# Kernel optimization log

Measured on AMD Instinct MI355X. Metric: run time of the kernel, lower is better.

The kernel has to match this reference:

```python
import jax, jax.numpy as jnp
import numpy as np

N_ATOM_BASIS = 128
MAX_Z = 100
N_GAUSSIANS = 25
N_FILTERS = 128
R_CUTOFF = 5.0


def ssp(x):
    # shifted softplus: log(0.5*exp(x) + 0.5)
    return jax.nn.softplus(x) - jnp.log(2.0).astype(x.dtype)


def setup_inputs() -> dict:
    key = jax.random.key(0)
    ks = jax.random.split(key, 12)
    N, K = 20000, 48
    dR = jax.random.uniform(ks[0], (N, K), jnp.float32) * R_CUTOFF
    Z = jax.random.randint(ks[1], (N,), 0, MAX_Z, jnp.int32)
    neighbor_idx = jax.random.randint(ks[2], (N, K), 0, N + 1, jnp.int32)  # idx == N is padding
    s = 1.0 / np.sqrt(N_ATOM_BASIS)
    return {
        "dR": dR,
        "Z": Z,
        "neighbor_idx": neighbor_idx,
        "embed": jax.random.normal(ks[3], (MAX_Z, N_ATOM_BASIS), jnp.float32),
        "in2f_w": jax.random.normal(ks[4], (N_ATOM_BASIS, N_FILTERS), jnp.float32) * s,
        "f1_w": jax.random.normal(ks[5], (N_GAUSSIANS, N_FILTERS), jnp.float32) * (1.0 / np.sqrt(N_GAUSSIANS)),
        "f1_b": jnp.zeros((N_FILTERS,), jnp.float32),
        "f2_w": jax.random.normal(ks[6], (N_FILTERS, N_FILTERS), jnp.float32) * s,
        "f2_b": jnp.zeros((N_FILTERS,), jnp.float32),
        "o1_w": jax.random.normal(ks[7], (N_FILTERS, N_ATOM_BASIS), jnp.float32) * s,
        "o1_b": jnp.zeros((N_ATOM_BASIS,), jnp.float32),
        "o2_w": jax.random.normal(ks[8], (N_ATOM_BASIS, N_ATOM_BASIS), jnp.float32) * s,
        "o2_b": jnp.zeros((N_ATOM_BASIS,), jnp.float32),
    }


def reference(dR, Z, neighbor_idx, embed, in2f_w, f1_w, f1_b, f2_w, f2_b,
              o1_w, o1_b, o2_w, o2_b):
    N = Z.shape[0]
    # atom embedding [N, 128]
    x = embed[Z]

    # gaussian smearing of distances [N, K, 25]
    offsets = jnp.linspace(0.0, R_CUTOFF, N_GAUSSIANS, dtype=jnp.float32)
    width = offsets[1] - offsets[0]
    coeff = -0.5 / (width * width)
    g = jnp.exp(coeff * jnp.square(dR[..., None] - offsets))

    # filter-generating network [N, K, F]
    W = ssp(g @ f1_w + f1_b) @ f2_w + f2_b

    # cosine cutoff and pairwise (padding) mask
    cut = 0.5 * (jnp.cos(dR * (jnp.pi / R_CUTOFF)) + 1.0) * (dR < R_CUTOFF)
    mask = (neighbor_idx < N).astype(jnp.float32)  # [N, K]
    W = W * (cut * mask)[..., None]

    # continuous-filter convolution: project, gather neighbors, weight, aggregate
    y = x @ in2f_w                                  # [N, F]
    idx_safe = jnp.where(neighbor_idx < N, neighbor_idx, 0)
    y_nb = y[idx_safe]                              # [N, K, F] gather
    agg = jnp.sum(y_nb * W, axis=1)                 # [N, F]

    # output network + residual
    v = ssp(agg @ o1_w + o1_b) @ o2_w + o2_b
    return x + v
```

## Files before the change

### kernel.cpp

```cpp
#include <hip/hip_runtime.h>
#include <hip/hip_fp16.h>
#include <math.h>

constexpr int F    = 128;
constexpr int KN   = 48;
constexpr int NG   = 25;
constexpr int TN   = 256;
constexpr int MAXZ = 100;

typedef _Float16 f16x8 __attribute__((ext_vector_type(8)));
typedef float    f32x4 __attribute__((ext_vector_type(4)));

__device__ __forceinline__ float ssp(float x) {
    return fmaxf(x, 0.0f) + __logf(fmaf(0.5f, __expf(-fabsf(x)), 0.5f));
}

__device__ __forceinline__ unsigned short f2h(float x) {
    return __half_as_ushort(__float2half_rn(x));
}
__device__ __forceinline__ __half2 u2h2(unsigned int u) {
    union { unsigned int u; __half2 h; } c; c.u = u; return c.h;
}

__global__ __launch_bounds__(256) void k_prep(
    const float* __restrict__ dR, const int* __restrict__ nbr,
    const int* __restrict__ Z,
    const float* __restrict__ f1w, const float* __restrict__ f1b,
    const float* __restrict__ f2w, const float* __restrict__ f2b,
    const float* __restrict__ o1w, const float* __restrict__ o2w,
    const float* __restrict__ embed, const float* __restrict__ in2f,
    unsigned int* __restrict__ params, unsigned int* __restrict__ tabp,
    unsigned int* __restrict__ yzp,
    unsigned short* __restrict__ o1f, unsigned short* __restrict__ o2f, int N)
{
    __shared__ float s0[F];
    __shared__ float s1[F];
    int bid = blockIdx.x;
    int tid = threadIdx.x;
    int nparam_blk = (N * KN + 255) >> 8;

    if (bid < nparam_blk) {
        int e = bid * 256 + tid;
        if (e < N * KN) {
            float d = dR[e];
            int   i = nbr[e];
            float u = d * ((float)TN / 5.0f);
            int   j = (int)u; j = (j > TN - 1) ? (TN - 1) : j;
            float fr = u - (float)j;
            unsigned int z = (i >= 0 && i < N) ? (unsigned int)Z[i] : (unsigned int)MAXZ;
            params[e] = ((unsigned int)f2h(fr) << 16) | ((unsigned int)j << 7) | z;
        }
        return;
    }
    bid -= nparam_blk;

    if (bid < TN + 1) {
        int j = bid, f = tid;
        float d = (float)j * (5.0f / (float)TN);
        constexpr float width = 5.0f / 24.0f;
        constexpr float coeff = -0.5f / (width * width);
        if (f < F) {
            float z = f1b[f];
            #pragma unroll
            for (int c = 0; c < NG; ++c) {
                float t = d - (float)c * width;
                z = fmaf(__expf(coeff * t * t), f1w[c * F + f], z);
            }
            s0[f] = ssp(z);
        }
        __syncthreads();
        if (f < F) {
            float w = f2b[f];
            #pragma unroll 8
            for (int c = 0; c < F; ++c)
                w = fmaf(s0[c], f2w[c * F + f], w);
            float cut = 0.5f * (cosf(d * 0.62831853071795864769f) + 1.0f);
            cut = (d < 5.0f) ? cut : 0.0f;
            s1[f] = w * cut;
        }
        __syncthreads();
        if (f < 64)
            tabp[j * 64 + f] = (unsigned int)f2h(s1[2 * f]) | ((unsigned int)f2h(s1[2 * f + 1]) << 16);
        return;
    }
    bid -= TN + 1;

    if (bid < 128) {
        int t = bid * 256 + tid;
        int e = t & 16383;
        int j = e & 7, l = (e >> 3) & 63, nt = (e >> 9) & 7, kt = e >> 12;
        int k = kt * 32 + ((l >> 4) << 3) + j;
        int col = nt * 16 + (l & 15);
        if (t < 16384) o1f[e] = f2h(o1w[k * F + col]);
        else           o2f[e] = f2h(o2w[k * F + col]);
        return;
    }
    bid -= 128;

    {
        int z = bid, f = tid;
        if (z < MAXZ) {
            if (f < F) s0[f] = embed[z * F + f];
            __syncthreads();
            if (f < F) {
                float acc = 0.f;
                #pragma unroll 8
                for (int c = 0; c < F; ++c)
                    acc = fmaf(s0[c], in2f[c * F + f], acc);
                s1[f] = acc;
            }
        } else {
            if (f < F) s1[f] = 0.f;
            __syncthreads();
        }
        __syncthreads();
        if (f < 64)
            yzp[z * 64 + f] = (unsigned int)f2h(s1[2 * f]) | ((unsigned int)f2h(s1[2 * f + 1]) << 16);
    }
}

__global__ __launch_bounds__(512, 4) void k_main(
    const unsigned int* __restrict__ params,
    const unsigned int* __restrict__ tabp,
    const unsigned int* __restrict__ yzp,
    const unsigned short* __restrict__ o1f, const float* __restrict__ o1b,
    const unsigned short* __restrict__ o2f, const float* __restrict__ o2b,
    const float* __restrict__ embed, const int* __restrict__ Z,
    float* __restrict__ out, int N, int ngroups)
{
    extern __shared__ unsigned int smem[];
    unsigned int*   tabL = smem;
    unsigned int*   aggL = smem + 16448;
    unsigned short* Us   = (unsigned short*)(smem + 16448 + 1024);

    int tid  = threadIdx.x;
    int wid  = tid >> 6;
    int lane = tid & 63;
    int lr   = lane & 15;
    int lg   = lane >> 4;

    for (int m = tid; m < (TN + 1) * 64; m += 512)
        tabL[m] = tabp[m];
    __syncthreads();

    for (int g = blockIdx.x; g < ngroups; g += gridDim.x) {
        int n0 = g * 16;

        int aA = wid * 2, aB = aA + 1;
        int nA = n0 + aA, nB = n0 + aB;
        float a0 = 0.f, a1 = 0.f, b0 = 0.f, b1 = 0.f;
        if (nA < N) {
            int mB = (nB < N) ? nB : nA;
            int baseA = __builtin_amdgcn_readfirstlane(nA) * KN;
            int baseB = __builtin_amdgcn_readfirstlane(mB) * KN;
            #pragma unroll
            for (int c = 0; c < 4; ++c) {
                __half2 pacA = u2h2(0u);
                __half2 pacB = u2h2(0u);
                #pragma unroll 4
                for (int k2 = 0; k2 < 12; ++k2) {
                    int k = c * 12 + k2;
                    unsigned int pA = params[baseA + k];
                    unsigned int pB = params[baseB + k];

                    __half2 frA = u2h2((pA & 0xFFFF0000u) | (pA >> 16));
                    __half2 frB = u2h2((pB & 0xFFFF0000u) | (pB >> 16));
                    unsigned int jbA = (pA & 0x7F80u) << 1;
                    unsigned int jbB = (pB & 0x7F80u) << 1;
                    unsigned int zbA = (pA & 0x7Fu) << 8;
                    unsigned int zbB = (pB & 0x7Fu) << 8;

                    const unsigned int* rA = (const unsigned int*)((const char*)tabL + jbA);
                    const unsigned int* rB = (const unsigned int*)((const char*)tabL + jbB);
                    __half2 tA0 = u2h2(rA[lane]);
                    __half2 tA1 = u2h2(rA[lane + 64]);
                    __half2 tB0 = u2h2(rB[lane]);
                    __half2 tB1 = u2h2(rB[lane + 64]);
                    __half2 yA  = u2h2(*(const unsigned int*)((const char*)yzp + zbA + (lane << 2)));
                    __half2 yB  = u2h2(*(const unsigned int*)((const char*)yzp + zbB + (lane << 2)));

                    __half2 wA = __hfma2(frA, __hsub2(tA1, tA0), tA0);
                    __half2 wB = __hfma2(frB, __hsub2(tB1, tB0), tB0);
                    pacA = __hfma2(wA, yA, pacA);
                    pacB = __hfma2(wB, yB, pacB);
                }
                float2 fa = __half22float2(pacA); a0 += fa.x; a1 += fa.y;
                float2 fb = __half22float2(pacB); b0 += fb.x; b1 += fb.y;
            }
        }
        aggL[aA * 64 + (lane ^ (aA << 2))] = (unsigned int)f2h(a0) | ((unsigned int)f2h(a1) << 16);
        aggL[aB * 64 + (lane ^ (aB << 2))] = (unsigned int)f2h(b0) | ((unsigned int)f2h(b1) << 16);
        __syncthreads();

        f32x4 c1 = {0.f, 0.f, 0.f, 0.f};
        #pragma unroll
        for (int kt = 0; kt < 4; ++kt) {
            f16x8 b = *reinterpret_cast<const f16x8*>(o1f + (((kt * 8 + wid) * 64 + lane) << 3));
            const char* ap = (const char*)aggL + lr * 256 + ((kt * 64 + lg * 16) ^ (lr << 4));
            f16x8 a = *reinterpret_cast<const f16x8*>(ap);
            c1 = __builtin_amdgcn_mfma_f32_16x16x32_f16(a, b, c1, 0, 0, 0);
        }
        int fcol = wid * 16 + lr;
        float bv1 = o1b[fcol];
        #pragma unroll
        for (int jr = 0; jr < 4; ++jr) {
            int r = lg * 4 + jr;
            float u = ssp(c1[jr] + bv1);
            Us[r * F + (fcol ^ (r << 3))] = f2h(u);
        }
        __syncthreads();

        f32x4 c2 = {0.f, 0.f, 0.f, 0.f};
        #pragma unroll
        for (int kt = 0; kt < 4; ++kt) {
            f16x8 b = *reinterpret_cast<const f16x8*>(o2f + (((kt * 8 + wid) * 64 + lane) << 3));
            f16x8 a = *reinterpret_cast<const f16x8*>(&Us[lr * F + ((kt * 32 + lg * 8) ^ (lr << 3))]);
            c2 = __builtin_amdgcn_mfma_f32_16x16x32_f16(a, b, c2, 0, 0, 0);
        }
        float bv2 = o2b[fcol];
        #pragma unroll
        for (int jr = 0; jr < 4; ++jr) {
            int r = lg * 4 + jr;
            int n = n0 + r;
            if (n < N) {
                float x = embed[Z[n] * F + fcol];
                out[n * F + fcol] = x + c2[jr] + bv2;
            }
        }
    }
}

extern "C" void kernel_launch(void* const* d_in, const int* in_sizes, int n_in,
                              void* d_out, int out_size, void* d_ws, size_t ws_size,
                              hipStream_t stream) {
    const float* dR    = (const float*)d_in[0];
    const int*   Z     = (const int*)  d_in[1];
    const int*   nbr   = (const int*)  d_in[2];
    const float* embed = (const float*)d_in[3];
    const float* in2f  = (const float*)d_in[4];
    const float* f1w   = (const float*)d_in[5];
    const float* f1b   = (const float*)d_in[6];
    const float* f2w   = (const float*)d_in[7];
    const float* f2b   = (const float*)d_in[8];
    const float* o1w   = (const float*)d_in[9];
    const float* o1b   = (const float*)d_in[10];
    const float* o2w   = (const float*)d_in[11];
    const float* o2b   = (const float*)d_in[12];

    int N = in_sizes[1];

    char* wp = (char*)d_ws;
    unsigned int*   params = (unsigned int*)wp;   wp += (size_t)N * KN * 4;
    unsigned int*   tabp   = (unsigned int*)wp;   wp += (size_t)(TN + 1) * 64 * 4;
    unsigned int*   yzp    = (unsigned int*)wp;   wp += (size_t)(MAXZ + 1) * 64 * 4;
    unsigned short* o1f    = (unsigned short*)wp; wp += 16384 * 2;
    unsigned short* o2f    = (unsigned short*)wp;

    int nparam_blk = (N * KN + 255) / 256;
    int grid_prep  = nparam_blk + (TN + 1) + 128 + (MAXZ + 1);

    int ngroups   = (N + 15) / 16;
    int grid_main = (ngroups < 512) ? ngroups : 512;
    int lds_main  = (TN + 1) * 64 * 4 + 4096 + 4096;

    (void)hipFuncSetAttribute((const void*)k_main,
                              hipFuncAttributeMaxDynamicSharedMemorySize, lds_main);

    k_prep<<<grid_prep, 256, 0, stream>>>(dR, nbr, Z, f1w, f1b, f2w, f2b,
                                          o1w, o2w, embed, in2f,
                                          params, tabp, yzp, o1f, o2f, N);
    k_main<<<grid_main, 512, lds_main, stream>>>(params, tabp, yzp,
                                                 o1f, o1b, o2f, o2b,
                                                 embed, Z, (float*)d_out,
                                                 N, ngroups);
}
```

Measured before the change: 41.82 us.

## Fuse neighbor param packing into main kernel and shrink interpolation table

The per-pair packing of distance fraction, table index and neighbor species moves out of the prep kernel. Each wave now computes it in registers inside the main kernel, one lane per neighbor, and broadcasts it with readlane. This removes the write and re-read of the N*K params buffer in global memory. The filter lookup table drops from 256 to 176 bins, which cuts LDS use so the launch bounds can allow 6 blocks per CU with a 768-block grid. The coarser table may lower interpolation accuracy, and the per-neighbor gathers of Z now happen inside the main kernel.

```diff
diff --git a/kernel.cpp b/kernel.cpp
--- a/kernel.cpp
+++ b/kernel.cpp
@@ -5,7 +5,7 @@
 constexpr int F    = 128;
 constexpr int KN   = 48;
 constexpr int NG   = 25;
-constexpr int TN   = 256;
+constexpr int TN   = 176;
 constexpr int MAXZ = 100;
 
 typedef _Float16 f16x8 __attribute__((ext_vector_type(8)));
@@ -23,36 +23,17 @@
 }
 
 __global__ __launch_bounds__(256) void k_prep(
-    const float* __restrict__ dR, const int* __restrict__ nbr,
-    const int* __restrict__ Z,
     const float* __restrict__ f1w, const float* __restrict__ f1b,
     const float* __restrict__ f2w, const float* __restrict__ f2b,
     const float* __restrict__ o1w, const float* __restrict__ o2w,
     const float* __restrict__ embed, const float* __restrict__ in2f,
-    unsigned int* __restrict__ params, unsigned int* __restrict__ tabp,
-    unsigned int* __restrict__ yzp,
+    unsigned int* __restrict__ tabp, unsigned int* __restrict__ yzp,
     unsigned short* __restrict__ o1f, unsigned short* __restrict__ o2f, int N)
 {
     __shared__ float s0[F];
     __shared__ float s1[F];
     int bid = blockIdx.x;
     int tid = threadIdx.x;
-    int nparam_blk = (N * KN + 255) >> 8;
-
-    if (bid < nparam_blk) {
-        int e = bid * 256 + tid;
-        if (e < N * KN) {
-            float d = dR[e];
-            int   i = nbr[e];
-            float u = d * ((float)TN / 5.0f);
-            int   j = (int)u; j = (j > TN - 1) ? (TN - 1) : j;
-            float fr = u - (float)j;
-            unsigned int z = (i >= 0 && i < N) ? (unsigned int)Z[i] : (unsigned int)MAXZ;
-            params[e] = ((unsigned int)f2h(fr) << 16) | ((unsigned int)j << 7) | z;
-        }
-        return;
-    }
-    bid -= nparam_blk;
 
     if (bid < TN + 1) {
         int j = bid, f = tid;
@@ -119,19 +100,20 @@
     }
 }
 
-__global__ __launch_bounds__(512, 4) void k_main(
-    const unsigned int* __restrict__ params,
+__global__ __launch_bounds__(512, 6) void k_main(
+    const float* __restrict__ dR, const int* __restrict__ nbr,
+    const int* __restrict__ Z,
     const unsigned int* __restrict__ tabp,
     const unsigned int* __restrict__ yzp,
     const unsigned short* __restrict__ o1f, const float* __restrict__ o1b,
     const unsigned short* __restrict__ o2f, const float* __restrict__ o2b,
-    const float* __restrict__ embed, const int* __restrict__ Z,
+    const float* __restrict__ embed,
     float* __restrict__ out, int N, int ngroups)
 {
     extern __shared__ unsigned int smem[];
     unsigned int*   tabL = smem;
-    unsigned int*   aggL = smem + 16448;
-    unsigned short* Us   = (unsigned short*)(smem + 16448 + 1024);
+    unsigned int*   aggL = smem + 11328;
+    unsigned short* Us   = (unsigned short*)(smem + 11328 + 1024);
 
     int tid  = threadIdx.x;
     int wid  = tid >> 6;
@@ -151,24 +133,42 @@
         float a0 = 0.f, a1 = 0.f, b0 = 0.f, b1 = 0.f;
         if (nA < N) {
             int mB = (nB < N) ? nB : nA;
-            int baseA = __builtin_amdgcn_readfirstlane(nA) * KN;
-            int baseB = __builtin_amdgcn_readfirstlane(mB) * KN;
+
+            unsigned int pA = 0, pB = 0;
+            if (lane < KN) {
+                float dA = dR[nA * KN + lane];
+                int   iA = nbr[nA * KN + lane];
+                float uA = dA * ((float)TN / 5.0f);
+                int   jA = (int)uA; jA = (jA > TN - 1) ? (TN - 1) : jA;
+                float fA = uA - (float)jA;
+                unsigned int zA = (iA >= 0 && iA < N) ? (unsigned int)Z[iA] : (unsigned int)MAXZ;
+                pA = ((unsigned int)f2h(fA) << 16) | ((unsigned int)jA << 7) | zA;
+
+                float dB = dR[mB * KN + lane];
+                int   iB = nbr[mB * KN + lane];
+                float uB = dB * ((float)TN / 5.0f);
+                int   jB = (int)uB; jB = (jB > TN - 1) ? (TN - 1) : jB;
+                float fB = uB - (float)jB;
+                unsigned int zB = (iB >= 0 && iB < N) ? (unsigned int)Z[iB] : (unsigned int)MAXZ;
+                pB = ((unsigned int)f2h(fB) << 16) | ((unsigned int)jB << 7) | zB;
+            }
+
             #pragma unroll
             for (int c = 0; c < 4; ++c) {
                 __half2 pacA = u2h2(0u);
                 __half2 pacB = u2h2(0u);
-                #pragma unroll 4
+                #pragma unroll
                 for (int k2 = 0; k2 < 12; ++k2) {
                     int k = c * 12 + k2;
-                    unsigned int pA = params[baseA + k];
-                    unsigned int pB = params[baseB + k];
-
-                    __half2 frA = u2h2((pA & 0xFFFF0000u) | (pA >> 16));
-                    __half2 frB = u2h2((pB & 0xFFFF0000u) | (pB >> 16));
-                    unsigned int jbA = (pA & 0x7F80u) << 1;
-                    unsigned int jbB = (pB & 0x7F80u) << 1;
-                    unsigned int zbA = (pA & 0x7Fu) << 8;
-                    unsigned int zbB = (pB & 0x7Fu) << 8;
+                    unsigned int qA = (unsigned int)__builtin_amdgcn_readlane((int)pA, k);
+                    unsigned int qB = (unsigned int)__builtin_amdgcn_readlane((int)pB, k);
+
+                    __half2 frA = u2h2((qA & 0xFFFF0000u) | (qA >> 16));
+                    __half2 frB = u2h2((qB & 0xFFFF0000u) | (qB >> 16));
+                    unsigned int jbA = (qA & 0x7F80u) << 1;
+                    unsigned int jbB = (qB & 0x7F80u) << 1;
+                    unsigned int zbA = (qA & 0x7Fu) << 8;
+                    unsigned int zbB = (qB & 0x7Fu) << 8;
 
                     const unsigned int* rA = (const unsigned int*)((const char*)tabL + jbA);
                     const unsigned int* rB = (const unsigned int*)((const char*)tabL + jbB);
@@ -250,27 +250,24 @@
     int N = in_sizes[1];
 
     char* wp = (char*)d_ws;
-    unsigned int*   params = (unsigned int*)wp;   wp += (size_t)N * KN * 4;
-    unsigned int*   tabp   = (unsigned int*)wp;   wp += (size_t)(TN + 1) * 64 * 4;
-    unsigned int*   yzp    = (unsigned int*)wp;   wp += (size_t)(MAXZ + 1) * 64 * 4;
-    unsigned short* o1f    = (unsigned short*)wp; wp += 16384 * 2;
-    unsigned short* o2f    = (unsigned short*)wp;
-
-    int nparam_blk = (N * KN + 255) / 256;
-    int grid_prep  = nparam_blk + (TN + 1) + 128 + (MAXZ + 1);
+    unsigned int*   tabp = (unsigned int*)wp;   wp += (size_t)(TN + 1) * 64 * 4;
+    unsigned int*   yzp  = (unsigned int*)wp;   wp += (size_t)(MAXZ + 1) * 64 * 4;
+    unsigned short* o1f  = (unsigned short*)wp; wp += 16384 * 2;
+    unsigned short* o2f  = (unsigned short*)wp;
+
+    int grid_prep = (TN + 1) + 128 + (MAXZ + 1);
 
     int ngroups   = (N + 15) / 16;
-    int grid_main = (ngroups < 512) ? ngroups : 512;
+    int grid_main = (ngroups < 768) ? ngroups : 768;
     int lds_main  = (TN + 1) * 64 * 4 + 4096 + 4096;
 
     (void)hipFuncSetAttribute((const void*)k_main,
                               hipFuncAttributeMaxDynamicSharedMemorySize, lds_main);
 
-    k_prep<<<grid_prep, 256, 0, stream>>>(dR, nbr, Z, f1w, f1b, f2w, f2b,
-                                          o1w, o2w, embed, in2f,
-                                          params, tabp, yzp, o1f, o2f, N);
-    k_main<<<grid_main, 512, lds_main, stream>>>(params, tabp, yzp,
+    k_prep<<<grid_prep, 256, 0, stream>>>(f1w, f1b, f2w, f2b, o1w, o2w,
+                                          embed, in2f, tabp, yzp, o1f, o2f, N);
+    k_main<<<grid_main, 512, lds_main, stream>>>(dR, nbr, Z, tabp, yzp,
                                                  o1f, o1b, o2f, o2b,
-                                                 embed, Z, (float*)d_out,
+                                                 embed, (float*)d_out,
                                                  N, ngroups);
 }
```

Result: faster. 36.81 us, median of 2 (-12.0%).
